# Optimization experiments

Hardware: AMD Instinct MI355X
Metric: run time of the kernel (lower is better)

## Reference

```python
import jax, jax.numpy as jnp
import numpy as np

B, T, CH_IN = 4096, 8, 2048
C, N, K = 1024, 512, 5  # chennel, prototype length, n_prototypes/classes
EPS = 1e-8


def setup_inputs() -> dict:
    key = jax.random.key(0)
    ks = jax.random.split(key, 14)
    rn = lambda k, s: jax.random.normal(k, s, dtype=jnp.float32)
    return {
        "x": rn(ks[0], (B, T, CH_IN)),
        "static": rn(ks[1], (K, CH_IN, N)),
        "Wk": rn(ks[2], (C, CH_IN)) * 0.02, "bk": rn(ks[3], (C,)) * 0.02,
        "Wv": rn(ks[4], (C, CH_IN)) * 0.02, "bv": rn(ks[5], (C,)) * 0.02,
        "WEk": rn(ks[6], (C, CH_IN)) * 0.02, "bEk": rn(ks[7], (C,)) * 0.02,
        "WEv": rn(ks[8], (C, CH_IN)) * 0.02, "bEv": rn(ks[9], (C,)) * 0.02,
        "Ww": rn(ks[10], (1, C)) * 0.02, "bw": rn(ks[11], (1,)) * 0.02,
        "Wout": rn(ks[12], (K, 2 * C)) * 0.02, "bout": rn(ks[13], (K,)) * 0.02,
    }


def reference(x, static, Wk, bk, Wv, bv, WEk, bEk, WEv, bEv, Ww, bw, Wout, bout):
    # last frame only: [B, ch_in]
    x_last = x[:, -1, :]
    # 1x1 convs on a length-1 sequence == plain linear layers
    k = x_last @ Wk.T + bk  # [B, C]
    v = x_last @ Wv.T + bv  # [B, C]
    # project all 5 static prototypes at once: [K, C, N]
    Ek = jnp.einsum('ci,kin->kcn', WEk, static) + bEk[None, :, None]
    Ev = jnp.einsum('ci,kin->kcn', WEv, static) + bEv[None, :, None]
    # cosine similarity along channel dim (torch eps=1e-8)
    kn = k / jnp.maximum(jnp.linalg.norm(k, axis=1, keepdims=True), EPS)
    Ekn = Ek / jnp.maximum(jnp.linalg.norm(Ek, axis=1, keepdims=True), EPS)
    sim = jnp.einsum('bc,kcn->bkn', kn, Ekn)          # [B, K, N]
    w = jax.nn.softmax(sim, axis=-1)                  # softmax over prototypes' N entries
    # weighted sum of Ev per prototype -> feature_E [B, C, K]
    feature_E = jnp.einsum('kcn,bkn->bck', Ev, w)
    # scalar gate per prototype via conv2_1_W, then sigmoid
    fw = jax.nn.sigmoid(jnp.einsum('c,bck->bk', Ww[0], feature_E) + bw[0])  # [B, K]
    fE = jnp.einsum('bck,bk->bc', feature_E, fw)      # [B, C]
    out = jax.nn.relu(jnp.concatenate([v, fE], axis=1))  # [B, 2C]
    out = out @ Wout.T + bout                          # [B, K]
    return out[:, :, None]                             # [B, K, 1] matching torch conv1d output
```

## Files before the change

kernel.cpp:

```cpp
#include <hip/hip_runtime.h>
#include <hip/hip_bf16.h>

#define BB 4096
#define TT 8
#define CHIN 2048
#define CC 1024
#define NN 512
#define KK 5
#define KN (KK*NN)

typedef __bf16 bf16x8 __attribute__((ext_vector_type(8)));
typedef float  f32x4  __attribute__((ext_vector_type(4)));

#define BM 256
#define BN 256

__device__ __forceinline__ void gload_lds16(const __hip_bfloat16* g, __hip_bfloat16* l) {
    __builtin_amdgcn_global_load_lds(
        (__attribute__((address_space(1))) void*)const_cast<__hip_bfloat16*>(g),
        (__attribute__((address_space(3))) void*)l, 16, 0, 0);
}

__device__ __forceinline__ void stage_half(const __hip_bfloat16* __restrict__ g, int ldg,
                                           __hip_bfloat16* l, int tid)
{
    #pragma unroll
    for (int q = 0; q < 2; ++q) {
        const int P   = q * 8192 + tid * 16;
        const int row = P >> 7;
        const int bc  = (P & 127) ^ ((row & 7) << 4);
        gload_lds16(g + (size_t)row * ldg + (bc >> 1),
                    (__hip_bfloat16*)((char*)l + P));
    }
}

__device__ __forceinline__ bf16x8 lds_read_swz(const __hip_bfloat16* base, int row, int kbyte)
{
    int off = row * 128 + kbyte;
    off ^= (row & 7) << 4;
    return *(const bf16x8*)((const char*)base + off);
}

__device__ __forceinline__ int xcd_remap()
{
    const int gx = gridDim.x, gy = gridDim.y, gz = gridDim.z;
    const int lin = blockIdx.x + gx * (blockIdx.y + gy * blockIdx.z);
    const int nwg = gx * gy * gz;
    return (lin & 7) * (nwg >> 3) + (lin >> 3);
}

__device__ __forceinline__ void gemm8p_body(
    const __hip_bfloat16* __restrict__ Ag, int lda,
    const __hip_bfloat16* __restrict__ Bg, int ldb,
    float* __restrict__ Cmat, int ldc,
    int ntiles,
    const float* __restrict__ bias_col,
    int bm, int bn)
{
    __shared__ __align__(16) __hip_bfloat16 As[2][BM * 64];
    __shared__ __align__(16) __hip_bfloat16 Bs[2][BN * 64];

    const int tid  = threadIdx.x;
    const int wave = tid >> 6;
    const int lane = tid & 63;
    const int wrow = (wave >> 2) * 128;
    const int wcol = (wave & 3) * 64;
    const int fr   = lane & 15;
    const int kb0  = (lane >> 4) * 16;

    const __hip_bfloat16* Arow = Ag + (size_t)bm * lda;
    const __hip_bfloat16* Brow = Bg + (size_t)bn * ldb;

    f32x4 acc[8][4];
    #pragma unroll
    for (int i = 0; i < 8; ++i)
        #pragma unroll
        for (int j = 0; j < 4; ++j)
            acc[i][j] = {0.f, 0.f, 0.f, 0.f};

    bf16x8 a[4][2];
    bf16x8 bfr[4][2];

    stage_half(Arow,                       lda, &As[0][0],        tid);
    stage_half(Arow + (size_t)128 * lda,   lda, &As[0][128 * 64], tid);
    stage_half(Brow,                       ldb, &Bs[0][0],        tid);
    stage_half(Brow + (size_t)128 * ldb,   ldb, &Bs[0][128 * 64], tid);
    if (ntiles > 1) {
        stage_half(Brow + 64,                     ldb, &Bs[1][0],        tid);
        stage_half(Brow + (size_t)128 * ldb + 64, ldb, &Bs[1][128 * 64], tid);
        asm volatile("s_waitcnt vmcnt(4)" ::: "memory");
    } else {
        asm volatile("s_waitcnt vmcnt(0)" ::: "memory");
    }
    __builtin_amdgcn_s_barrier();
    __builtin_amdgcn_sched_barrier(0);

    for (int T = 0; T < ntiles; ++T) {
        const __hip_bfloat16* Abuf = &As[T & 1][0];
        const __hip_bfloat16* Bbuf = &Bs[T & 1][0];

        #pragma unroll
        for (int i = 0; i < 4; ++i)
            #pragma unroll
            for (int k2 = 0; k2 < 2; ++k2)
                a[i][k2] = lds_read_swz(Abuf, wrow + i * 16 + fr, k2 * 64 + kb0);
        #pragma unroll
        for (int j = 0; j < 2; ++j)
            #pragma unroll
            for (int k2 = 0; k2 < 2; ++k2)
                bfr[j][k2] = lds_read_swz(Bbuf, wcol + j * 16 + fr, k2 * 64 + kb0);
        if (T + 1 < ntiles)
            stage_half(Arow + (size_t)(T + 1) * 64, lda, &As[(T + 1) & 1][0], tid);
        __builtin_amdgcn_s_barrier();
        asm volatile("s_waitcnt lgkmcnt(0)" ::: "memory");
        __builtin_amdgcn_sched_barrier(0);
        __builtin_amdgcn_s_setprio(1);
        #pragma unroll
        for (int i = 0; i < 4; ++i)
            #pragma unroll
            for (int j = 0; j < 2; ++j)
                #pragma unroll
                for (int k2 = 0; k2 < 2; ++k2)
                    acc[i][j] = __builtin_amdgcn_mfma_f32_16x16x32_bf16(
                        a[i][k2], bfr[j][k2], acc[i][j], 0, 0, 0);
        __builtin_amdgcn_s_setprio(0);
        __builtin_amdgcn_s_barrier();
        __builtin_amdgcn_sched_barrier(0);

        #pragma unroll
        for (int j = 2; j < 4; ++j)
            #pragma unroll
            for (int k2 = 0; k2 < 2; ++k2)
                bfr[j][k2] = lds_read_swz(Bbuf, wcol + j * 16 + fr, k2 * 64 + kb0);
        if (T + 1 < ntiles)
            stage_half(Arow + (size_t)128 * lda + (size_t)(T + 1) * 64, lda,
                       &As[(T + 1) & 1][128 * 64], tid);
        __builtin_amdgcn_s_barrier();
        asm volatile("s_waitcnt lgkmcnt(0)" ::: "memory");
        __builtin_amdgcn_sched_barrier(0);
        __builtin_amdgcn_s_setprio(1);
        #pragma unroll
        for (int i = 0; i < 4; ++i)
            #pragma unroll
            for (int j = 2; j < 4; ++j)
                #pragma unroll
                for (int k2 = 0; k2 < 2; ++k2)
                    acc[i][j] = __builtin_amdgcn_mfma_f32_16x16x32_bf16(
                        a[i][k2], bfr[j][k2], acc[i][j], 0, 0, 0);
        __builtin_amdgcn_s_setprio(0);
        __builtin_amdgcn_s_barrier();
        __builtin_amdgcn_sched_barrier(0);

        #pragma unroll
        for (int i = 0; i < 4; ++i)
            #pragma unroll
            for (int k2 = 0; k2 < 2; ++k2)
                a[i][k2] = lds_read_swz(Abuf, wrow + 64 + i * 16 + fr, k2 * 64 + kb0);
        if (T + 2 < ntiles)
            stage_half(Brow + (size_t)(T + 2) * 64, ldb, &Bs[T & 1][0], tid);
        __builtin_amdgcn_s_barrier();
        asm volatile("s_waitcnt lgkmcnt(0)" ::: "memory");
        __builtin_amdgcn_sched_barrier(0);
        __builtin_amdgcn_s_setprio(1);
        #pragma unroll
        for (int i = 0; i < 4; ++i)
            #pragma unroll
            for (int j = 2; j < 4; ++j)
                #pragma unroll
                for (int k2 = 0; k2 < 2; ++k2)
                    acc[i + 4][j] = __builtin_amdgcn_mfma_f32_16x16x32_bf16(
                        a[i][k2], bfr[j][k2], acc[i + 4][j], 0, 0, 0);
        __builtin_amdgcn_s_setprio(0);
        __builtin_amdgcn_s_barrier();
        __builtin_amdgcn_sched_barrier(0);

        if (T + 2 < ntiles) {
            stage_half(Brow + (size_t)128 * ldb + (size_t)(T + 2) * 64, ldb,
                       &Bs[T & 1][128 * 64], tid);
            asm volatile("s_waitcnt vmcnt(4)" ::: "memory");
        } else if (T + 1 < ntiles) {
            asm volatile("s_waitcnt vmcnt(0)" ::: "memory");
        }
        __builtin_amdgcn_s_barrier();
        __builtin_amdgcn_sched_barrier(0);
        __builtin_amdgcn_s_setprio(1);
        #pragma unroll
        for (int i = 0; i < 4; ++i)
            #pragma unroll
            for (int j = 0; j < 2; ++j)
                #pragma unroll
                for (int k2 = 0; k2 < 2; ++k2)
                    acc[i + 4][j] = __builtin_amdgcn_mfma_f32_16x16x32_bf16(
                        a[i][k2], bfr[j][k2], acc[i + 4][j], 0, 0, 0);
        __builtin_amdgcn_s_setprio(0);
        __builtin_amdgcn_s_barrier();
        __builtin_amdgcn_sched_barrier(0);
    }

    const int quad = lane >> 4;
    #pragma unroll
    for (int i = 0; i < 8; ++i) {
        #pragma unroll
        for (int j = 0; j < 4; ++j) {
            const int col = bn + wcol + j * 16 + fr;
            const float bc = bias_col ? bias_col[col] : 0.f;
            #pragma unroll
            for (int r = 0; r < 4; ++r) {
                const int row = bm + wrow + i * 16 + quad * 4 + r;
                Cmat[(size_t)row * ldc + col] = acc[i][j][r] + bc;
            }
        }
    }
}

__global__ __launch_bounds__(512) void gemm8p_dual(
    const __hip_bfloat16* __restrict__ A0, const __hip_bfloat16* __restrict__ B0,
    float* __restrict__ C0, const float* __restrict__ bias0, int mt0,
    const __hip_bfloat16* __restrict__ A1, const __hip_bfloat16* __restrict__ B1,
    float* __restrict__ C1, const float* __restrict__ bias1)
{
    const int W  = xcd_remap();
    const int bx = W % gridDim.x;
    const int by = W / gridDim.x;
    const bool s = by >= mt0;
    gemm8p_body(s ? A1 : A0, CHIN, s ? B1 : B0, CHIN,
                s ? C1 : C0, 2 * CC, CHIN / 64,
                s ? bias1 : bias0,
                (s ? by - mt0 : by) * BM, bx * BN);
}

__global__ __launch_bounds__(512) void gemm8p(
    const __hip_bfloat16* __restrict__ A, int lda,
    const __hip_bfloat16* __restrict__ BT, int ldb,
    float* __restrict__ C, int ldc, int ntiles,
    const float* __restrict__ bias)
{
    const int W  = xcd_remap();
    const int bx = W % gridDim.x;
    const int by = W / gridDim.x;
    gemm8p_body(A, lda, BT, ldb, C, ldc, ntiles, bias, by * BM, bx * BN);
}

__global__ __launch_bounds__(512) void gemm8p_splitk(
    const __hip_bfloat16* __restrict__ A, int lda,
    const __hip_bfloat16* __restrict__ BT, int ldb,
    float* __restrict__ C0, float* __restrict__ C1, int ldc, int khalf_tiles)
{
    const int W   = xcd_remap();
    const int gxy = gridDim.x * gridDim.y;
    const int z   = W / gxy;
    const int rem = W % gxy;
    const int bx  = rem % gridDim.x;
    const int by  = rem / gridDim.x;
    gemm8p_body(A + (size_t)z * khalf_tiles * 64, lda,
                BT + (size_t)z * khalf_tiles * 64, ldb,
                z ? C1 : C0, ldc, khalf_tiles, nullptr,
                by * BM, bx * BN);
}

#define WG ((CC*CHIN)/4)
#define XG ((BB*CHIN)/4)
#define PREP_BLOCKS ((4*WG + XG + 1024) / 256)

__device__ __forceinline__ void store_bf4(__hip_bfloat16* dst, float4 vv) {
    union { __hip_bfloat16 h[4]; unsigned long long u; } pk;
    pk.h[0] = (__hip_bfloat16)vv.x; pk.h[1] = (__hip_bfloat16)vv.y;
    pk.h[2] = (__hip_bfloat16)vv.z; pk.h[3] = (__hip_bfloat16)vv.w;
    *(unsigned long long*)dst = pk.u;
}

__global__ __launch_bounds__(256) void prep_flat(
    const float* __restrict__ Wk, const float* __restrict__ Wv,
    const float* __restrict__ WEk, const float* __restrict__ WEv,
    const float* __restrict__ x,
    const float* __restrict__ bk, const float* __restrict__ bv,
    const float* __restrict__ bEk, const float* __restrict__ bEv,
    __hip_bfloat16* __restrict__ Wkvb, __hip_bfloat16* __restrict__ WEkvb,
    __hip_bfloat16* __restrict__ xb,
    float* __restrict__ bkv, float* __restrict__ bEkv)
{
    const int gidx = blockIdx.x * 256 + threadIdx.x;
    if (gidx < 4 * WG) {
        const int mat = gidx >> 19;
        const int off = (gidx & (WG - 1)) * 4;
        const float* src = (mat == 0) ? Wk : (mat == 1) ? Wv : (mat == 2) ? WEk : WEv;
        __hip_bfloat16* dst = (mat < 2) ? (Wkvb + (size_t)mat * (CC * CHIN))
                                        : (WEkvb + (size_t)(mat - 2) * (CC * CHIN));
        store_bf4(dst + off, *(const float4*)(src + off));
    } else if (gidx < 4 * WG + XG) {
        const int off = (gidx - 4 * WG) * 4;
        const int b = off >> 11;
        const int i = off & (CHIN - 1);
        store_bf4(xb + off, *(const float4*)(x + ((size_t)b * TT + TT - 1) * CHIN + i));
    } else {
        const int off = (gidx - 4 * WG - XG) * 4;
        #pragma unroll
        for (int e = 0; e < 4; ++e) {
            const int t = off + e;
            if (t < 2 * CC) bkv[t]  = (t < CC) ? bk[t] : bv[t - CC];
            else { const int u2 = t - 2 * CC; bEkv[u2] = (u2 < CC) ? bEk[u2] : bEv[u2 - CC]; }
        }
    }
}

__global__ void transpose_static(const float* __restrict__ st,
                                 __hip_bfloat16* __restrict__ stT)
{
    __shared__ float tile[32][33];
    const int k  = blockIdx.z;
    const int i0 = blockIdx.x * 32;
    const int n0 = blockIdx.y * 32;
    const int tx = threadIdx.x, ty = threadIdx.y;
    #pragma unroll
    for (int r = 0; r < 32; r += 8)
        tile[ty + r][tx] = st[((size_t)k * CHIN + i0 + ty + r) * NN + n0 + tx];
    __syncthreads();
    #pragma unroll
    for (int r = 0; r < 32; r += 8)
        stT[((size_t)k * NN + n0 + ty + r) * CHIN + i0 + tx] = (__hip_bfloat16)tile[tx][ty + r];
}

__global__ void transpose_bf16(const __hip_bfloat16* __restrict__ in,
                               __hip_bfloat16* __restrict__ outp)
{
    __shared__ __hip_bfloat16 tile[32][33];
    const int c0  = blockIdx.x * 32;
    const int kn0 = blockIdx.y * 32;
    const int tx = threadIdx.x, ty = threadIdx.y;
    #pragma unroll
    for (int r = 0; r < 32; r += 8)
        tile[ty + r][tx] = in[(size_t)(kn0 + ty + r) * CC + c0 + tx];
    __syncthreads();
    #pragma unroll
    for (int r = 0; r < 32; r += 8)
        outp[(size_t)(c0 + ty + r) * KN + kn0 + tx] = tile[tx][ty + r];
}

__global__ __launch_bounds__(256) void norm_prep_E(const float* __restrict__ Ekv,
                                                   const float* __restrict__ Ww,
                                                   __hip_bfloat16* __restrict__ EknT,
                                                   float* __restrict__ g,
                                                   __hip_bfloat16* __restrict__ EvT)
{
    const int kn = blockIdx.x;
    const float* pk = Ekv + (size_t)kn * (2 * CC);
    const float* pv = pk + CC;
    float s2 = 0.f, sg = 0.f;
    for (int c = threadIdx.x; c < CC; c += 256) {
        const float ek = pk[c]; s2 += ek * ek;
        const float ev = pv[c]; sg += Ww[c] * ev;
        EvT[(size_t)kn * CC + c] = (__hip_bfloat16)ev;
    }
    #pragma unroll
    for (int o = 32; o > 0; o >>= 1) { s2 += __shfl_down(s2, o, 64); sg += __shfl_down(sg, o, 64); }
    __shared__ float r2[4], rg[4];
    if ((threadIdx.x & 63) == 0) { r2[threadIdx.x >> 6] = s2; rg[threadIdx.x >> 6] = sg; }
    __syncthreads();
    const float tot = r2[0] + r2[1] + r2[2] + r2[3];
    const float inv = 1.f / fmaxf(sqrtf(tot), 1e-8f);
    for (int c = threadIdx.x; c < CC; c += 256)
        EknT[(size_t)kn * CC + c] = (__hip_bfloat16)(pk[c] * inv);
    if (threadIdx.x == 0) g[kn] = rg[0] + rg[1] + rg[2] + rg[3];
}

__global__ __launch_bounds__(256) void rownorm(const float* __restrict__ in, int in_ld,
                                               __hip_bfloat16* __restrict__ out, int cols)
{
    const int row = blockIdx.x;
    const float* p = in + (size_t)row * in_ld;
    float s = 0.f;
    for (int c = threadIdx.x; c < cols; c += 256) { float v = p[c]; s += v * v; }
    #pragma unroll
    for (int o = 32; o > 0; o >>= 1) s += __shfl_down(s, o, 64);
    __shared__ float red[4];
    if ((threadIdx.x & 63) == 0) red[threadIdx.x >> 6] = s;
    __syncthreads();
    const float tot = red[0] + red[1] + red[2] + red[3];
    const float inv = 1.f / fmaxf(sqrtf(tot), 1e-8f);
    for (int c = threadIdx.x; c < cols; c += 256)
        out[(size_t)row * cols + c] = (__hip_bfloat16)(p[c] * inv);
}

__global__ __launch_bounds__(64) void softmax_u(const float* __restrict__ sim,
                                                const float* __restrict__ g,
                                                const float* __restrict__ bw,
                                                __hip_bfloat16* __restrict__ u)
{
    const int bk = blockIdx.x;
    const int b = bk / KK, k = bk % KK;
    const float* sp = sim + (size_t)b * KN + k * NN;
    const float* gp = g + k * NN;
    const int lane = threadIdx.x;

    float vals[8];
    float m = -1e30f;
    #pragma unroll
    for (int j = 0; j < 8; ++j) { vals[j] = sp[lane + 64 * j]; m = fmaxf(m, vals[j]); }
    #pragma unroll
    for (int o = 32; o > 0; o >>= 1) m = fmaxf(m, __shfl_xor(m, o, 64));
    float sum = 0.f;
    #pragma unroll
    for (int j = 0; j < 8; ++j) { vals[j] = expf(vals[j] - m); sum += vals[j]; }
    #pragma unroll
    for (int o = 32; o > 0; o >>= 1) sum += __shfl_xor(sum, o, 64);
    const float inv = 1.f / sum;
    float dot = 0.f;
    #pragma unroll
    for (int j = 0; j < 8; ++j) { vals[j] *= inv; dot += vals[j] * gp[lane + 64 * j]; }
    #pragma unroll
    for (int o = 32; o > 0; o >>= 1) dot += __shfl_xor(dot, o, 64);
    const float fw = 1.f / (1.f + expf(-(dot + bw[0])));
    __hip_bfloat16* up = u + (size_t)b * KN + k * NN;
    #pragma unroll
    for (int j = 0; j < 8; ++j) up[lane + 64 * j] = (__hip_bfloat16)(vals[j] * fw);
}

__global__ __launch_bounds__(256) void final_out(const float* __restrict__ kv,
                                                 const float* __restrict__ fE0,
                                                 const float* __restrict__ fE1,
                                                 const float* __restrict__ Wout,
                                                 const float* __restrict__ bout,
                                                 float* __restrict__ out)
{
    const int b = blockIdx.x;
    const float* vp = kv + (size_t)b * (2 * CC) + CC;
    float acc[KK] = {0.f, 0.f, 0.f, 0.f, 0.f};
    for (int c = threadIdx.x; c < CC; c += 256) {
        const float rv = fmaxf(vp[c], 0.f);
        const float rf = fmaxf(fE0[(size_t)b * CC + c] + fE1[(size_t)b * CC + c], 0.f);
        #pragma unroll
        for (int kk = 0; kk < KK; ++kk)
            acc[kk] += Wout[kk * 2 * CC + c] * rv
                     + Wout[kk * 2 * CC + CC + c] * rf;
    }
    __shared__ float red[KK][4];
    const int lane = threadIdx.x & 63, wave = threadIdx.x >> 6;
    #pragma unroll
    for (int kk = 0; kk < KK; ++kk) {
        float s = acc[kk];
        #pragma unroll
        for (int o = 32; o > 0; o >>= 1) s += __shfl_down(s, o, 64);
        if (lane == 0) red[kk][wave] = s;
    }
    __syncthreads();
    if (threadIdx.x < KK) {
        float s = red[threadIdx.x][0] + red[threadIdx.x][1]
                + red[threadIdx.x][2] + red[threadIdx.x][3];
        out[(size_t)b * KK + threadIdx.x] = s + bout[threadIdx.x];
    }
}

extern "C" void kernel_launch(void* const* d_in, const int* in_sizes, int n_in,
                              void* d_out, int out_size, void* d_ws, size_t ws_size,
                              hipStream_t stream)
{
    const float* x    = (const float*)d_in[0];
    const float* stat = (const float*)d_in[1];
    const float* Wk   = (const float*)d_in[2];
    const float* bk   = (const float*)d_in[3];
    const float* Wv   = (const float*)d_in[4];
    const float* bv   = (const float*)d_in[5];
    const float* WEk  = (const float*)d_in[6];
    const float* bEk  = (const float*)d_in[7];
    const float* WEv  = (const float*)d_in[8];
    const float* bEv  = (const float*)d_in[9];
    const float* Ww   = (const float*)d_in[10];
    const float* bw   = (const float*)d_in[11];
    const float* Wout = (const float*)d_in[12];
    const float* bout = (const float*)d_in[13];
    float* out = (float*)d_out;
    char* ws = (char*)d_ws;

    __hip_bfloat16* xb      = (__hip_bfloat16*)(ws + 0);
    __hip_bfloat16* Wkvb    = (__hip_bfloat16*)(ws + 16777216);
    __hip_bfloat16* WEkvb   = (__hip_bfloat16*)(ws + 25165824);
    __hip_bfloat16* staticT = (__hip_bfloat16*)(ws + 33554432);
    float*          Ekv     = (float*)(ws + 44040192);
    __hip_bfloat16* EknT    = (__hip_bfloat16*)(ws + 65011712);
    __hip_bfloat16* EvT     = (__hip_bfloat16*)(ws + 70254592);
    __hip_bfloat16* EvC     = (__hip_bfloat16*)(ws + 75497472);
    float*          g       = (float*)(ws + 80740352);
    float*          kv      = (float*)(ws + 80750592);
    __hip_bfloat16* kn      = (__hip_bfloat16*)(ws + 114305024);
    float*          sim     = (float*)(ws + 122693632);
    __hip_bfloat16* u       = (__hip_bfloat16*)(ws + 164636672);
    float*          fE      = (float*)(ws + 185608192);
    float*          bkv     = (float*)(ws + 202385408);
    float*          bEkv    = (float*)(ws + 202393600);
    float*          fE2     = (float*)(ws + 202401792);

    prep_flat<<<PREP_BLOCKS, 256, 0, stream>>>(
        Wk, Wv, WEk, WEv, x, bk, bv, bEk, bEv, Wkvb, WEkvb, xb, bkv, bEkv);
    transpose_static<<<dim3(CHIN / 32, NN / 32, KK), dim3(32, 8), 0, stream>>>(stat, staticT);

    gemm8p_dual<<<dim3(2 * CC / BN, KN / BM + BB / BM), 512, 0, stream>>>(
        staticT, WEkvb, Ekv, bEkv, KN / BM,
        xb, Wkvb, kv, bkv);
    norm_prep_E<<<KN, 256, 0, stream>>>(Ekv, Ww, EknT, g, EvT);
    transpose_bf16<<<dim3(CC / 32, KN / 32), dim3(32, 8), 0, stream>>>(EvT, EvC);
    rownorm<<<BB, 256, 0, stream>>>(kv, 2 * CC, kn, CC);
    gemm8p<<<dim3(KN / BN, BB / BM), 512, 0, stream>>>(
        kn, CC, EknT, CC, sim, KN, CC / 64, nullptr);
    softmax_u<<<BB * KK, 64, 0, stream>>>(sim, g, bw, u);
    gemm8p_splitk<<<dim3(CC / BN, BB / BM, 2), 512, 0, stream>>>(
        u, KN, EvC, KN, fE, fE2, CC, (KN / 2) / 64);
    final_out<<<BB, 256, 0, stream>>>(kv, fE, fE2, Wout, bout, out);
}
```

Baseline: 548.9 us.

## Restructure GEMM prefetch schedule, fuse Ev transpose, and pack softmax blocks

The GEMM main loop now double-buffers both A and B two tiles ahead in quarter-sized stages, and precomputes the swizzled LDS offsets once per thread instead of on every read. The Ev transpose reads fp32 Ekv directly, which drops the intermediate EvT bf16 buffer and its write and read traffic. softmax_u packs four 64-thread rows into each 256-thread block, cutting the launch to a quarter as many blocks. The reworked prefetch ordering and vmcnt thresholds are timing-sensitive and risk changing load/compute overlap or LDS hazards.

```diff
diff --git a/kernel.cpp b/kernel.cpp
--- a/kernel.cpp
+++ b/kernel.cpp
@@ -21,24 +21,14 @@
         (__attribute__((address_space(3))) void*)l, 16, 0, 0);
 }
 
-__device__ __forceinline__ void stage_half(const __hip_bfloat16* __restrict__ g, int ldg,
-                                           __hip_bfloat16* l, int tid)
-{
-    #pragma unroll
-    for (int q = 0; q < 2; ++q) {
-        const int P   = q * 8192 + tid * 16;
-        const int row = P >> 7;
-        const int bc  = (P & 127) ^ ((row & 7) << 4);
-        gload_lds16(g + (size_t)row * ldg + (bc >> 1),
-                    (__hip_bfloat16*)((char*)l + P));
-    }
-}
-
-__device__ __forceinline__ bf16x8 lds_read_swz(const __hip_bfloat16* base, int row, int kbyte)
-{
-    int off = row * 128 + kbyte;
-    off ^= (row & 7) << 4;
-    return *(const bf16x8*)((const char*)base + off);
+__device__ __forceinline__ void stage_q(const __hip_bfloat16* __restrict__ g, int ldg,
+                                        __hip_bfloat16* l, int tid)
+{
+    const int P   = tid * 16;
+    const int row = P >> 7;
+    const int bc  = (P & 127) ^ ((row & 7) << 4);
+    gload_lds16(g + (size_t)row * ldg + (bc >> 1),
+                (__hip_bfloat16*)((char*)l + P));
 }
 
 __device__ __forceinline__ int xcd_remap()
@@ -71,6 +61,13 @@
     const __hip_bfloat16* Arow = Ag + (size_t)bm * lda;
     const __hip_bfloat16* Brow = Bg + (size_t)bn * ldb;
 
+    const int rA = wrow + fr, rB = wcol + fr;
+    const int swA = (rA & 7) << 4, swB = (rB & 7) << 4;
+    const int offA0 = rA * 128 + ((kb0     ) ^ swA);
+    const int offA1 = rA * 128 + ((kb0 + 64) ^ swA);
+    const int offB0 = rB * 128 + ((kb0     ) ^ swB);
+    const int offB1 = rB * 128 + ((kb0 + 64) ^ swB);
+
     f32x4 acc[8][4];
     #pragma unroll
     for (int i = 0; i < 8; ++i)
@@ -79,16 +76,23 @@
             acc[i][j] = {0.f, 0.f, 0.f, 0.f};
 
     bf16x8 a[4][2];
-    bf16x8 bfr[4][2];
-
-    stage_half(Arow,                       lda, &As[0][0],        tid);
-    stage_half(Arow + (size_t)128 * lda,   lda, &As[0][128 * 64], tid);
-    stage_half(Brow,                       ldb, &Bs[0][0],        tid);
-    stage_half(Brow + (size_t)128 * ldb,   ldb, &Bs[0][128 * 64], tid);
+    bf16x8 b01[2][2];
+    bf16x8 b23[2][2];
+
+    #pragma unroll
+    for (int q = 0; q < 4; ++q)
+        stage_q(Arow + (size_t)(64 * q) * lda, lda, &As[0][q * 4096], tid);
+    #pragma unroll
+    for (int q = 0; q < 4; ++q)
+        stage_q(Brow + (size_t)(64 * q) * ldb, ldb, &Bs[0][q * 4096], tid);
     if (ntiles > 1) {
-        stage_half(Brow + 64,                     ldb, &Bs[1][0],        tid);
-        stage_half(Brow + (size_t)128 * ldb + 64, ldb, &Bs[1][128 * 64], tid);
-        asm volatile("s_waitcnt vmcnt(4)" ::: "memory");
+        #pragma unroll
+        for (int q = 0; q < 4; ++q)
+            stage_q(Arow + (size_t)(64 * q) * lda + 64, lda, &As[1][q * 4096], tid);
+        #pragma unroll
+        for (int q = 0; q < 4; ++q)
+            stage_q(Brow + (size_t)(64 * q) * ldb + 64, ldb, &Bs[1][q * 4096], tid);
+        asm volatile("s_waitcnt vmcnt(8)" ::: "memory");
     } else {
         asm volatile("s_waitcnt vmcnt(0)" ::: "memory");
     }
@@ -96,21 +100,23 @@
     __builtin_amdgcn_sched_barrier(0);
 
     for (int T = 0; T < ntiles; ++T) {
-        const __hip_bfloat16* Abuf = &As[T & 1][0];
-        const __hip_bfloat16* Bbuf = &Bs[T & 1][0];
-
-        #pragma unroll
-        for (int i = 0; i < 4; ++i)
-            #pragma unroll
-            for (int k2 = 0; k2 < 2; ++k2)
-                a[i][k2] = lds_read_swz(Abuf, wrow + i * 16 + fr, k2 * 64 + kb0);
-        #pragma unroll
-        for (int j = 0; j < 2; ++j)
-            #pragma unroll
-            for (int k2 = 0; k2 < 2; ++k2)
-                bfr[j][k2] = lds_read_swz(Bbuf, wcol + j * 16 + fr, k2 * 64 + kb0);
-        if (T + 1 < ntiles)
-            stage_half(Arow + (size_t)(T + 1) * 64, lda, &As[(T + 1) & 1][0], tid);
+        const char* aB = (const char*)&As[T & 1][0];
+        const char* bB = (const char*)&Bs[T & 1][0];
+        const char* aK0 = aB + offA0; const char* aK1 = aB + offA1;
+        const char* bK0 = bB + offB0; const char* bK1 = bB + offB1;
+        const bool pf = (T + 2 < ntiles);
+        const int  kc = (T + 2) * 64;
+
+        #pragma unroll
+        for (int i = 0; i < 4; ++i) {
+            a[i][0] = *(const bf16x8*)(aK0 + i * 2048);
+            a[i][1] = *(const bf16x8*)(aK1 + i * 2048);
+        }
+        #pragma unroll
+        for (int j = 0; j < 2; ++j) {
+            b01[j][0] = *(const bf16x8*)(bK0 + j * 2048);
+            b01[j][1] = *(const bf16x8*)(bK1 + j * 2048);
+        }
         __builtin_amdgcn_s_barrier();
         asm volatile("s_waitcnt lgkmcnt(0)" ::: "memory");
         __builtin_amdgcn_sched_barrier(0);
@@ -122,19 +128,20 @@
                 #pragma unroll
                 for (int k2 = 0; k2 < 2; ++k2)
                     acc[i][j] = __builtin_amdgcn_mfma_f32_16x16x32_bf16(
-                        a[i][k2], bfr[j][k2], acc[i][j], 0, 0, 0);
+                        a[i][k2], b01[j][k2], acc[i][j], 0, 0, 0);
         __builtin_amdgcn_s_setprio(0);
         __builtin_amdgcn_s_barrier();
         __builtin_amdgcn_sched_barrier(0);
 
         #pragma unroll
-        for (int j = 2; j < 4; ++j)
-            #pragma unroll
-            for (int k2 = 0; k2 < 2; ++k2)
-                bfr[j][k2] = lds_read_swz(Bbuf, wcol + j * 16 + fr, k2 * 64 + kb0);
-        if (T + 1 < ntiles)
-            stage_half(Arow + (size_t)128 * lda + (size_t)(T + 1) * 64, lda,
-                       &As[(T + 1) & 1][128 * 64], tid);
+        for (int j = 0; j < 2; ++j) {
+            b23[j][0] = *(const bf16x8*)(bK0 + (j + 2) * 2048);
+            b23[j][1] = *(const bf16x8*)(bK1 + (j + 2) * 2048);
+        }
+        if (pf) {
+            stage_q(Arow + kc,                       lda, &As[T & 1][0],        tid);
+            stage_q(Arow + (size_t)128 * lda + kc,   lda, &As[T & 1][2 * 4096], tid);
+        }
         __builtin_amdgcn_s_barrier();
         asm volatile("s_waitcnt lgkmcnt(0)" ::: "memory");
         __builtin_amdgcn_sched_barrier(0);
@@ -142,42 +149,45 @@
         #pragma unroll
         for (int i = 0; i < 4; ++i)
             #pragma unroll
-            for (int j = 2; j < 4; ++j)
+            for (int j = 0; j < 2; ++j)
                 #pragma unroll
                 for (int k2 = 0; k2 < 2; ++k2)
-                    acc[i][j] = __builtin_amdgcn_mfma_f32_16x16x32_bf16(
-                        a[i][k2], bfr[j][k2], acc[i][j], 0, 0, 0);
+                    acc[i][j + 2] = __builtin_amdgcn_mfma_f32_16x16x32_bf16(
+                        a[i][k2], b23[j][k2], acc[i][j + 2], 0, 0, 0);
         __builtin_amdgcn_s_setprio(0);
         __builtin_amdgcn_s_barrier();
         __builtin_amdgcn_sched_barrier(0);
 
+        #pragma unroll
+        for (int i = 0; i < 4; ++i) {
+            a[i][0] = *(const bf16x8*)(aK0 + 8192 + i * 2048);
+            a[i][1] = *(const bf16x8*)(aK1 + 8192 + i * 2048);
+        }
+        if (pf) {
+            #pragma unroll
+            for (int q = 0; q < 4; ++q)
+                stage_q(Brow + (size_t)(64 * q) * ldb + kc, ldb, &Bs[T & 1][q * 4096], tid);
+        }
+        __builtin_amdgcn_s_barrier();
+        asm volatile("s_waitcnt lgkmcnt(0)" ::: "memory");
+        __builtin_amdgcn_sched_barrier(0);
+        __builtin_amdgcn_s_setprio(1);
         #pragma unroll
         for (int i = 0; i < 4; ++i)
             #pragma unroll
-            for (int k2 = 0; k2 < 2; ++k2)
-                a[i][k2] = lds_read_swz(Abuf, wrow + 64 + i * 16 + fr, k2 * 64 + kb0);
-        if (T + 2 < ntiles)
-            stage_half(Brow + (size_t)(T + 2) * 64, ldb, &Bs[T & 1][0], tid);
-        __builtin_amdgcn_s_barrier();
-        asm volatile("s_waitcnt lgkmcnt(0)" ::: "memory");
-        __builtin_amdgcn_sched_barrier(0);
-        __builtin_amdgcn_s_setprio(1);
-        #pragma unroll
-        for (int i = 0; i < 4; ++i)
-            #pragma unroll
-            for (int j = 2; j < 4; ++j)
+            for (int j = 0; j < 2; ++j)
                 #pragma unroll
                 for (int k2 = 0; k2 < 2; ++k2)
-                    acc[i + 4][j] = __builtin_amdgcn_mfma_f32_16x16x32_bf16(
-                        a[i][k2], bfr[j][k2], acc[i + 4][j], 0, 0, 0);
+                    acc[i + 4][j + 2] = __builtin_amdgcn_mfma_f32_16x16x32_bf16(
+                        a[i][k2], b23[j][k2], acc[i + 4][j + 2], 0, 0, 0);
         __builtin_amdgcn_s_setprio(0);
         __builtin_amdgcn_s_barrier();
         __builtin_amdgcn_sched_barrier(0);
 
-        if (T + 2 < ntiles) {
-            stage_half(Brow + (size_t)128 * ldb + (size_t)(T + 2) * 64, ldb,
-                       &Bs[T & 1][128 * 64], tid);
-            asm volatile("s_waitcnt vmcnt(4)" ::: "memory");
+        if (pf) {
+            stage_q(Arow + (size_t)64 * lda + kc,    lda, &As[T & 1][4096],     tid);
+            stage_q(Arow + (size_t)192 * lda + kc,   lda, &As[T & 1][3 * 4096], tid);
+            asm volatile("s_waitcnt vmcnt(8)" ::: "memory");
         } else if (T + 1 < ntiles) {
             asm volatile("s_waitcnt vmcnt(0)" ::: "memory");
         }
@@ -191,7 +201,7 @@
                 #pragma unroll
                 for (int k2 = 0; k2 < 2; ++k2)
                     acc[i + 4][j] = __builtin_amdgcn_mfma_f32_16x16x32_bf16(
-                        a[i][k2], bfr[j][k2], acc[i + 4][j], 0, 0, 0);
+                        a[i][k2], b01[j][k2], acc[i + 4][j], 0, 0, 0);
         __builtin_amdgcn_s_setprio(0);
         __builtin_amdgcn_s_barrier();
         __builtin_amdgcn_sched_barrier(0);
@@ -320,27 +330,26 @@
         stT[((size_t)k * NN + n0 + ty + r) * CHIN + i0 + tx] = (__hip_bfloat16)tile[tx][ty + r];
 }
 
-__global__ void transpose_bf16(const __hip_bfloat16* __restrict__ in,
-                               __hip_bfloat16* __restrict__ outp)
-{
-    __shared__ __hip_bfloat16 tile[32][33];
+__global__ void transpose_Ev(const float* __restrict__ Ekv,
+                             __hip_bfloat16* __restrict__ EvC)
+{
+    __shared__ float tile[32][33];
     const int c0  = blockIdx.x * 32;
     const int kn0 = blockIdx.y * 32;
     const int tx = threadIdx.x, ty = threadIdx.y;
     #pragma unroll
     for (int r = 0; r < 32; r += 8)
-        tile[ty + r][tx] = in[(size_t)(kn0 + ty + r) * CC + c0 + tx];
+        tile[ty + r][tx] = Ekv[(size_t)(kn0 + ty + r) * (2 * CC) + CC + c0 + tx];
     __syncthreads();
     #pragma unroll
     for (int r = 0; r < 32; r += 8)
-        outp[(size_t)(c0 + ty + r) * KN + kn0 + tx] = tile[tx][ty + r];
+        EvC[(size_t)(c0 + ty + r) * KN + kn0 + tx] = (__hip_bfloat16)tile[tx][ty + r];
 }
 
 __global__ __launch_bounds__(256) void norm_prep_E(const float* __restrict__ Ekv,
                                                    const float* __restrict__ Ww,
                                                    __hip_bfloat16* __restrict__ EknT,
-                                                   float* __restrict__ g,
-                                                   __hip_bfloat16* __restrict__ EvT)
+                                                   float* __restrict__ g)
 {
     const int kn = blockIdx.x;
     const float* pk = Ekv + (size_t)kn * (2 * CC);
@@ -348,8 +357,7 @@
     float s2 = 0.f, sg = 0.f;
     for (int c = threadIdx.x; c < CC; c += 256) {
         const float ek = pk[c]; s2 += ek * ek;
-        const float ev = pv[c]; sg += Ww[c] * ev;
-        EvT[(size_t)kn * CC + c] = (__hip_bfloat16)ev;
+        sg += Ww[c] * pv[c];
     }
     #pragma unroll
     for (int o = 32; o > 0; o >>= 1) { s2 += __shfl_down(s2, o, 64); sg += __shfl_down(sg, o, 64); }
@@ -381,16 +389,16 @@
         out[(size_t)row * cols + c] = (__hip_bfloat16)(p[c] * inv);
 }
 
-__global__ __launch_bounds__(64) void softmax_u(const float* __restrict__ sim,
-                                                const float* __restrict__ g,
-                                                const float* __restrict__ bw,
-                                                __hip_bfloat16* __restrict__ u)
-{
-    const int bk = blockIdx.x;
+__global__ __launch_bounds__(256) void softmax_u(const float* __restrict__ sim,
+                                                 const float* __restrict__ g,
+                                                 const float* __restrict__ bw,
+                                                 __hip_bfloat16* __restrict__ u)
+{
+    const int bk = blockIdx.x * 4 + (threadIdx.x >> 6);
     const int b = bk / KK, k = bk % KK;
     const float* sp = sim + (size_t)b * KN + k * NN;
     const float* gp = g + k * NN;
-    const int lane = threadIdx.x;
+    const int lane = threadIdx.x & 63;
 
     float vals[8];
     float m = -1e30f;
@@ -477,7 +485,6 @@
     __hip_bfloat16* staticT = (__hip_bfloat16*)(ws + 33554432);
     float*          Ekv     = (float*)(ws + 44040192);
     __hip_bfloat16* EknT    = (__hip_bfloat16*)(ws + 65011712);
-    __hip_bfloat16* EvT     = (__hip_bfloat16*)(ws + 70254592);
     __hip_bfloat16* EvC     = (__hip_bfloat16*)(ws + 75497472);
     float*          g       = (float*)(ws + 80740352);
     float*          kv      = (float*)(ws + 80750592);
@@ -496,12 +503,12 @@
     gemm8p_dual<<<dim3(2 * CC / BN, KN / BM + BB / BM), 512, 0, stream>>>(
         staticT, WEkvb, Ekv, bEkv, KN / BM,
         xb, Wkvb, kv, bkv);
-    norm_prep_E<<<KN, 256, 0, stream>>>(Ekv, Ww, EknT, g, EvT);
-    transpose_bf16<<<dim3(CC / 32, KN / 32), dim3(32, 8), 0, stream>>>(EvT, EvC);
+    norm_prep_E<<<KN, 256, 0, stream>>>(Ekv, Ww, EknT, g);
+    transpose_Ev<<<dim3(CC / 32, KN / 32), dim3(32, 8), 0, stream>>>(Ekv, EvC);
     rownorm<<<BB, 256, 0, stream>>>(kv, 2 * CC, kn, CC);
     gemm8p<<<dim3(KN / BN, BB / BM), 512, 0, stream>>>(
         kn, CC, EknT, CC, sim, KN, CC / 64, nullptr);
-    softmax_u<<<BB * KK, 64, 0, stream>>>(sim, g, bw, u);
+    softmax_u<<<BB * KK / 4, 256, 0, stream>>>(sim, g, bw, u);
     gemm8p_splitk<<<dim3(CC / BN, BB / BM, 2), 512, 0, stream>>>(
         u, KN, EvC, KN, fE, fE2, CC, (KN / 2) / 64);
     final_out<<<BB, 256, 0, stream>>>(kv, fE, fE2, Wout, bout, out);
```

After: 540.1 us. About the same (-1.6%).
